# Optimization experiments

Hardware: AMD Instinct MI355X
Metric: run time of the kernel (lower is better)

Reference implementation:

```python
import jax, jax.numpy as jnp
import numpy as np

B, N, C, H = 4, 1024, 768, 12
D = C // H
HID = 4 * C
SCALE = D ** -0.5
EPS = 1e-6


def layernorm(x, w, b):
    mu = jnp.mean(x, axis=-1, keepdims=True)
    var = jnp.mean(jnp.square(x - mu), axis=-1, keepdims=True)
    return (x - mu) * jax.lax.rsqrt(var + EPS) * w + b


def setup_inputs() -> dict:
    key = jax.random.key(0)
    ks = jax.random.split(key, 16)
    s = lambda fan_in: 1.0 / np.sqrt(fan_in)
    return {
        "x": jax.random.normal(ks[0], (B, N, C), jnp.float32),
        "physics_bias": jax.random.normal(ks[1], (B, N, N), jnp.float32),
        "qkv_w": jax.random.normal(ks[2], (C, 3 * C), jnp.float32) * s(C),
        "qkv_b": jnp.zeros((3 * C,), jnp.float32),
        "proj_w": jax.random.normal(ks[3], (C, C), jnp.float32) * s(C),
        "proj_b": jnp.zeros((C,), jnp.float32),
        "n1_w": jnp.ones((C,), jnp.float32),
        "n1_b": jnp.zeros((C,), jnp.float32),
        "n2_w": jnp.ones((C,), jnp.float32),
        "n2_b": jnp.zeros((C,), jnp.float32),
        "fc1_w": jax.random.normal(ks[4], (C, HID), jnp.float32) * s(C),
        "fc1_b": jnp.zeros((HID,), jnp.float32),
        "fc2_w": jax.random.normal(ks[5], (HID, C), jnp.float32) * s(HID),
        "fc2_b": jnp.zeros((C,), jnp.float32),
    }


def reference(x, physics_bias, qkv_w, qkv_b, proj_w, proj_b,
              n1_w, n1_b, n2_w, n2_b, fc1_w, fc1_b, fc2_w, fc2_b):
    # --- biased self-attention (pre-norm) ---
    h = layernorm(x, n1_w, n1_b)                         # [B,N,C]
    qkv = (h @ qkv_w + qkv_b).reshape(B, N, 3, H, D)     # [B,N,3,H,D]
    q, k, v = (qkv[:, :, i] for i in range(3))           # each [B,N,H,D]
    attn = jnp.einsum('bnhd,bmhd->bhnm', q, k) * SCALE   # [B,H,N,N]
    attn = attn + physics_bias[:, None, :, :]            # additive physics bias
    attn = jax.nn.softmax(attn, axis=-1)
    o = jnp.einsum('bhnm,bmhd->bnhd', attn, v).reshape(B, N, C)
    x = x + (o @ proj_w + proj_b)
    # --- MLP (pre-norm) ---
    h = layernorm(x, n2_w, n2_b)
    h = jax.nn.gelu(h @ fc1_w + fc1_b, approximate=False)
    x = x + (h @ fc2_w + fc2_b)
    return x
```

## Files before the change

### kernel.cpp

```cpp
#include <hip/hip_runtime.h>
#include <hip/hip_bf16.h>
#include <cstdint>
#include <cstddef>

#define B_   4
#define N_   1024
#define C_   768
#define H_   12
#define D_   64
#define HID_ 3072
#define M_   4096

typedef __attribute__((ext_vector_type(8))) short short8;
typedef __attribute__((ext_vector_type(8))) unsigned short ushort8;
typedef __attribute__((ext_vector_type(4))) float f32x4;

__device__ __forceinline__ void gload16(const void* g, void* l) {
  __builtin_amdgcn_global_load_lds(
      (const __attribute__((address_space(1))) void*)g,
      (__attribute__((address_space(3))) void*)l, 16, 0, 0);
}

__device__ __forceinline__ unsigned short f2bf(float f) {
  __hip_bfloat16 h = __float2bfloat16(f);
  return __builtin_bit_cast(unsigned short, h);
}
__device__ __forceinline__ float bf2f(unsigned short u) {
  unsigned int x = ((unsigned int)u) << 16;
  return __builtin_bit_cast(float, x);
}
__device__ __forceinline__ float ex2(float x) {
  float r;
  asm("v_exp_f32 %0, %1" : "=v"(r) : "v"(x));
  return r;
}
__device__ __forceinline__ float frcp(float x) {
  float r;
  asm("v_rcp_f32 %0, %1" : "=v"(r) : "v"(x));
  return r;
}

__global__ __launch_bounds__(256) void wconv_all(
    const float* __restrict__ qkv_w, const float* __restrict__ proj_w,
    const float* __restrict__ fc1_w, const float* __restrict__ fc2_w,
    unsigned short* __restrict__ wt_qkv, unsigned short* __restrict__ wt_proj,
    unsigned short* __restrict__ wt_fc1, unsigned short* __restrict__ wt_fc2) {
  __shared__ float tile[32][33];
  const int bid = blockIdx.x;
  const float* W;
  unsigned short* Wt;
  int K, Nn, bx, by;
  if (bid < 1728) {
    W = qkv_w; Wt = wt_qkv; K = 768; Nn = 2304;
    bx = bid % 72; by = bid / 72;
  } else if (bid < 1728 + 576) {
    const int i = bid - 1728;
    W = proj_w; Wt = wt_proj; K = 768; Nn = 768;
    bx = i % 24; by = i / 24;
  } else if (bid < 1728 + 576 + 2304) {
    const int i = bid - (1728 + 576);
    W = fc1_w; Wt = wt_fc1; K = 768; Nn = 3072;
    bx = i % 96; by = i / 96;
  } else {
    const int i = bid - (1728 + 576 + 2304);
    W = fc2_w; Wt = wt_fc2; K = 3072; Nn = 768;
    bx = i % 24; by = i / 24;
  }
  const int tx = threadIdx.x & 31, ty = threadIdx.x >> 5;
  const int n0 = bx * 32, k0 = by * 32;
#pragma unroll
  for (int i = 0; i < 32; i += 8)
    tile[ty + i][tx] = W[(size_t)(k0 + ty + i) * Nn + n0 + tx];
  __syncthreads();
#pragma unroll
  for (int i = 0; i < 32; i += 8)
    Wt[(size_t)(n0 + ty + i) * K + k0 + tx] = f2bf(tile[tx][ty + i]);
}

__global__ __launch_bounds__(256) void ln_kernel(const float* __restrict__ x,
                                                 const float* __restrict__ w,
                                                 const float* __restrict__ b,
                                                 unsigned short* __restrict__ out) {
  __shared__ float sbuf[8];
  const int row = blockIdx.x;
  const int t = threadIdx.x;
  const float* xr = x + (size_t)row * C_;
  float v0 = xr[t], v1 = xr[t + 256], v2 = xr[t + 512];
  float s = v0 + v1 + v2;
  float ss = v0 * v0 + v1 * v1 + v2 * v2;
#pragma unroll
  for (int m = 32; m >= 1; m >>= 1) {
    s += __shfl_xor(s, m);
    ss += __shfl_xor(ss, m);
  }
  const int wave = t >> 6, lane = t & 63;
  if (lane == 0) { sbuf[wave] = s; sbuf[4 + wave] = ss; }
  __syncthreads();
  s = sbuf[0] + sbuf[1] + sbuf[2] + sbuf[3];
  ss = sbuf[4] + sbuf[5] + sbuf[6] + sbuf[7];
  const float mu = s * (1.f / C_);
  const float var = ss * (1.f / C_) - mu * mu;
  const float rstd = rsqrtf(var + 1e-6f);
  unsigned short* o = out + (size_t)row * C_;
  o[t]       = f2bf((v0 - mu) * rstd * w[t]       + b[t]);
  o[t + 256] = f2bf((v1 - mu) * rstd * w[t + 256] + b[t + 256]);
  o[t + 512] = f2bf((v2 - mu) * rstd * w[t + 512] + b[t + 512]);
}

template <int MF, bool GELU, bool RES, bool OUTF, bool OUTB>
__global__ __launch_bounds__(256) void gemm_bt(const unsigned short* __restrict__ A,
                                               const unsigned short* __restrict__ Bt,
                                               const float* __restrict__ bias,
                                               const float* __restrict__ res,
                                               float* __restrict__ outF,
                                               unsigned short* __restrict__ outB,
                                               int M, int Nn, int K) {
  __shared__ unsigned short As[3][MF * 32 * 32];
  __shared__ unsigned short Bs[3][128 * 32];
  const int t = threadIdx.x;
  const int lane = t & 63;
  const int wave = t >> 6;
  const int wm = wave >> 1, wn = wave & 1;
  const int r15 = lane & 15, g = lane >> 4;

  constexpr int SPX = (MF == 4) ? 4 : 8;
  constexpr int LGS = (MF == 4) ? 2 : 3;
  const int orig = blockIdx.y * gridDim.x + blockIdx.x;
  const int xcd = orig & 7;
  const int j = orig >> 3;
  const int bm = xcd * SPX + (j & (SPX - 1));
  const int bn = j >> LGS;

  f32x4 acc[MF][4];
#pragma unroll
  for (int m = 0; m < MF; ++m)
#pragma unroll
    for (int n = 0; n < 4; ++n) acc[m][n] = (f32x4){0.f, 0.f, 0.f, 0.f};

  const int srow = t >> 2;
  const int schunk = (t & 3) ^ ((t >> 3) & 3);
  const unsigned short* ga0 = A + (size_t)(bm * (MF * 32) + srow) * K + schunk * 8;
  const unsigned short* gb0 = Bt + (size_t)(bn * 128 + srow) * K + schunk * 8;

#define GSTAGE(kt_, buf_)                                                  \
  {                                                                        \
    const unsigned short* ga = ga0 + (kt_)*32;                             \
    const unsigned short* gb = gb0 + (kt_)*32;                             \
    gload16(ga, (char*)As[buf_] + wave * 1024);                            \
    if constexpr (MF == 4)                                                 \
      gload16(ga + (size_t)64 * K, (char*)As[buf_] + wave * 1024 + 4096);  \
    gload16(gb, (char*)Bs[buf_] + wave * 1024);                            \
    gload16(gb + (size_t)64 * K, (char*)Bs[buf_] + wave * 1024 + 4096);    \
  }

  const int nk = K >> 5;
  GSTAGE(0, 0);
  GSTAGE(1, 1);

  int arow[MF], aoff[MF], boff[4];
#pragma unroll
  for (int m = 0; m < MF; ++m) {
    arow[m] = wm * (MF * 16) + m * 16 + r15;
    aoff[m] = arow[m] * 32 + (g ^ ((arow[m] >> 1) & 3)) * 8;
  }
#pragma unroll
  for (int n = 0; n < 4; ++n) {
    const int rn = wn * 64 + n * 16 + r15;
    boff[n] = rn * 32 + (g ^ ((rn >> 1) & 3)) * 8;
  }

  int rd = 0;
  for (int kt = 0; kt < nk; ++kt) {
    const int rem = nk - kt;
    if (rem >= 2) {
      if constexpr (MF == 4) asm volatile("s_waitcnt vmcnt(4)" ::: "memory");
      else                   asm volatile("s_waitcnt vmcnt(3)" ::: "memory");
    } else {
      asm volatile("s_waitcnt vmcnt(0)" ::: "memory");
    }
    __builtin_amdgcn_s_barrier();

    short8 af[MF], bf[4];
#pragma unroll
    for (int m = 0; m < MF; ++m)
      af[m] = *(const short8*)(As[rd] + aoff[m]);
#pragma unroll
    for (int n = 0; n < 4; ++n)
      bf[n] = *(const short8*)(Bs[rd] + boff[n]);

    if (kt + 2 < nk) {
      const int wr = (rd + 2 >= 3) ? rd - 1 : rd + 2;
      GSTAGE(kt + 2, wr);
    }

    asm volatile("s_waitcnt lgkmcnt(0)" ::: "memory");
    __builtin_amdgcn_sched_barrier(0);
    __builtin_amdgcn_s_setprio(1);
#pragma unroll
    for (int m = 0; m < MF; ++m)
#pragma unroll
      for (int n = 0; n < 4; ++n)
        acc[m][n] = __builtin_amdgcn_mfma_f32_16x16x32_bf16(af[m], bf[n], acc[m][n], 0, 0, 0);
    __builtin_amdgcn_s_setprio(0);
    rd = (rd == 2) ? 0 : rd + 1;
  }
#undef GSTAGE

#pragma unroll
  for (int m = 0; m < MF; ++m) {
#pragma unroll
    for (int n = 0; n < 4; ++n) {
#pragma unroll
      for (int r = 0; r < 4; ++r) {
        const int row = bm * (MF * 32) + wm * (MF * 16) + m * 16 + g * 4 + r;
        const int col = bn * 128 + wn * 64 + n * 16 + r15;
        float v = acc[m][n][r] + bias[col];
        if (GELU) v = 0.5f * v * (1.f + erff(v * 0.70710678118654752f));
        if (RES) v += res[(size_t)row * Nn + col];
        if (OUTF) outF[(size_t)row * Nn + col] = v;
        if (OUTB) outB[(size_t)row * Nn + col] = f2bf(v);
      }
    }
  }
}

__global__ __launch_bounds__(256) void attn_kernel(const unsigned short* __restrict__ qkv,
                                                   const float* __restrict__ pbias,
                                                   unsigned short* __restrict__ o) {
  __shared__ unsigned short Ks[2][64 * 64];
  __shared__ unsigned short Vt[2][64 * 64];
  __shared__ unsigned short Ps[4][16 * 64];
  const int t = threadIdx.x, lane = t & 63, wave = t >> 6;
  const int bh = blockIdx.y;
  const int b = bh / H_, h = bh % H_;
  const int q0 = blockIdx.x * 64;
  const int r15 = lane & 15, g = lane >> 4;
  const int qrow = q0 + wave * 16;
  const float LOG2E = 1.44269504088896f;
  const float QS = 0.125f * 1.44269504088896f;
  const int NT = N_ / 64;

  short8 aq[2];
  {
    const unsigned short* qp =
        qkv + (size_t)(b * N_ + qrow + r15) * (3 * C_) + h * D_ + g * 8;
    const ushort8 r0 = *(const ushort8*)qp;
    const ushort8 r1 = *(const ushort8*)(qp + 32);
#pragma unroll
    for (int jj = 0; jj < 8; ++jj) {
      aq[0][jj] = (short)f2bf(bf2f(r0[jj]) * QS);
      aq[1][jj] = (short)f2bf(bf2f(r1[jj]) * QS);
    }
  }
  short8 ones;
#pragma unroll
  for (int jj = 0; jj < 8; ++jj) ones[jj] = (short)0x3F80;

  f32x4 oacc[4], lacc;
#pragma unroll
  for (int n = 0; n < 4; ++n) oacc[n] = (f32x4){0.f, 0.f, 0.f, 0.f};
  lacc = (f32x4){0.f, 0.f, 0.f, 0.f};
  float m_run = -1e30f;

  const unsigned short* kbase = qkv + (size_t)b * N_ * (3 * C_) + C_ + h * D_;
  const unsigned short* vbase = qkv + (size_t)b * N_ * (3 * C_) + 2 * C_ + h * D_;
  const float* bq = pbias + (size_t)b * N_ * N_ + (size_t)(qrow + r15) * N_;

  const int krow = t >> 3;
  const int kchunk = (t & 7) ^ (krow & 7);
  const int vp = t & 31;
  const int vq = t >> 5;
  const int vkey = vp * 2, vd0 = vq * 8;

#define KSTAGE(kb_, nb_)                                                       \
  {                                                                            \
    const unsigned short* kg =                                                 \
        kbase + (size_t)((kb_)*64 + krow) * (3 * C_) + kchunk * 8;             \
    gload16(kg, (char*)Ks[nb_] + wave * 1024);                                 \
    gload16(kg + (size_t)32 * (3 * C_), (char*)Ks[nb_] + wave * 1024 + 4096);  \
  }

#define VWRITE(nb_, va_, vb_)                                                        \
  {                                                                                  \
    char* vdst = (char*)Vt[nb_];                                                     \
    _Pragma("unroll") for (int jj = 0; jj < 8; ++jj) {                               \
      const int d = vd0 + jj;                                                        \
      const unsigned int pack =                                                      \
          (unsigned int)(va_)[jj] | ((unsigned int)(vb_)[jj] << 16);                 \
      *(unsigned int*)(vdst + d * 128 + (((vp >> 2) ^ (d & 7)) << 4) +               \
                       (vp & 3) * 4) = pack;                                         \
    }                                                                                \
  }

  KSTAGE(0, 0);
  f32x4 biasA[4], biasB[4];
  {
    const unsigned short* vg = vbase + (size_t)vkey * (3 * C_) + vd0;
    const ushort8 va0 = *(const ushort8*)vg;
    const ushort8 vb0 = *(const ushort8*)(vg + 3 * C_);
#pragma unroll
    for (int n = 0; n < 4; ++n) biasA[n] = *(const f32x4*)(bq + n * 16 + g * 4);
#pragma unroll
    for (int n = 0; n < 4; ++n) biasB[n] = *(const f32x4*)(bq + 64 + n * 16 + g * 4);
    VWRITE(0, va0, vb0);
  }

#define ABODY(kb_, BS)                                                             \
  {                                                                                \
    const int cur_ = (kb_)&1;                                                      \
    asm volatile("s_waitcnt lgkmcnt(0)" ::: "memory");                             \
    asm volatile("s_waitcnt vmcnt(4)" ::: "memory");                               \
    __builtin_amdgcn_s_barrier();                                                  \
    ushort8 va, vb2;                                                               \
    const bool more = (kb_) + 1 < NT;                                              \
    if (more) {                                                                    \
      KSTAGE((kb_) + 1, cur_ ^ 1);                                                 \
      const unsigned short* vg =                                                   \
          vbase + (size_t)(((kb_) + 1) * 64 + vkey) * (3 * C_) + vd0;              \
      va = *(const ushort8*)vg;                                                    \
      vb2 = *(const ushort8*)(vg + 3 * C_);                                        \
    }                                                                              \
    const unsigned short* Ksc = Ks[cur_];                                          \
    f32x4 sacc[4];                                                                 \
    _Pragma("unroll") for (int n = 0; n < 4; ++n)                                  \
        sacc[n] = (f32x4){0.f, 0.f, 0.f, 0.f};                                     \
    __builtin_amdgcn_s_setprio(1);                                                 \
    _Pragma("unroll") for (int kk = 0; kk < 2; ++kk) {                             \
      _Pragma("unroll") for (int n = 0; n < 4; ++n) {                              \
        short8 bk = *(const short8*)(Ksc + (n * 16 + r15) * 64 +                   \
                                     (((kk * 4 + g) ^ (r15 & 7)) << 3));           \
        sacc[n] =                                                                  \
            __builtin_amdgcn_mfma_f32_16x16x32_bf16(bk, aq[kk], sacc[n], 0, 0, 0); \
      }                                                                            \
    }                                                                              \
    __builtin_amdgcn_s_setprio(0);                                                 \
    float p[4][4];                                                                 \
    float tm = -3e38f;                                                             \
    _Pragma("unroll") for (int n = 0; n < 4; ++n) {                                \
      _Pragma("unroll") for (int r = 0; r < 4; ++r) {                              \
        p[n][r] = fmaf(BS[n][r], LOG2E, sacc[n][r]);                               \
        tm = fmaxf(tm, p[n][r]);                                                   \
      }                                                                            \
    }                                                                              \
    __builtin_amdgcn_sched_barrier(0);                                             \
    {                                                                              \
      const float* bsrc = bq + (((kb_) + 2 < NT ? (kb_) + 2 : NT - 1) << 6);       \
      _Pragma("unroll") for (int n = 0; n < 4; ++n)                                \
          BS[n] = *(const f32x4*)(bsrc + n * 16 + g * 4);                          \
    }                                                                              \
    __builtin_amdgcn_sched_barrier(0);                                             \
    tm = fmaxf(tm, __shfl_xor(tm, 16));                                            \
    tm = fmaxf(tm, __shfl_xor(tm, 32));                                            \
    const int need = (tm > m_run + 8.0f);                                          \
    if (__any(need)) {                                                             \
      const float mn = fmaxf(m_run, tm);                                           \
      const float corr = ex2(m_run - mn);                                          \
      m_run = mn;                                                                  \
      float cr[4];                                                                 \
      _Pragma("unroll") for (int r = 0; r < 4; ++r)                                \
          cr[r] = __shfl(corr, g * 4 + r);                                         \
      _Pragma("unroll") for (int r = 0; r < 4; ++r) {                              \
        lacc[r] *= cr[r];                                                          \
        _Pragma("unroll") for (int n = 0; n < 4; ++n) oacc[n][r] *= cr[r];         \
      }                                                                            \
    }                                                                              \
    _Pragma("unroll") for (int n = 0; n < 4; ++n) {                                \
      _Pragma("unroll") for (int r = 0; r < 4; ++r)                                \
          p[n][r] = ex2(p[n][r] - m_run);                                          \
    }                                                                              \
    unsigned short* Psw = Ps[wave];                                                \
    _Pragma("unroll") for (int n = 0; n < 4; ++n) {                                \
      _Pragma("unroll") for (int r = 0; r < 4; ++r) {                              \
        const int col = n * 16 + g * 4 + r;                                        \
        Psw[r15 * 64 + (((col >> 3) ^ (r15 & 7)) << 3) + (col & 7)] =              \
            f2bf(p[n][r]);                                                         \
      }                                                                            \
    }                                                                              \
    const unsigned short* Vtc = Vt[cur_];                                          \
    __builtin_amdgcn_s_setprio(1);                                                 \
    _Pragma("unroll") for (int kk = 0; kk < 2; ++kk) {                             \
      short8 ap =                                                                  \
          *(const short8*)(Psw + r15 * 64 + (((kk * 4 + g) ^ (r15 & 7)) << 3));    \
      lacc = __builtin_amdgcn_mfma_f32_16x16x32_bf16(ap, ones, lacc, 0, 0, 0);     \
      _Pragma("unroll") for (int n = 0; n < 4; ++n) {                              \
        short8 bv = *(const short8*)(Vtc + (n * 16 + r15) * 64 +                   \
                                     (((kk * 4 + g) ^ (r15 & 7)) << 3));           \
        oacc[n] =                                                                  \
            __builtin_amdgcn_mfma_f32_16x16x32_bf16(ap, bv, oacc[n], 0, 0, 0);     \
      }                                                                            \
    }                                                                              \
    __builtin_amdgcn_s_setprio(0);                                                 \
    if (more) { VWRITE(cur_ ^ 1, va, vb2); }                                       \
  }

  for (int kb2 = 0; kb2 < NT; kb2 += 2) {
    ABODY(kb2, biasA);
    ABODY(kb2 + 1, biasB);
  }
#undef ABODY
#undef KSTAGE
#undef VWRITE

  float rl[4];
#pragma unroll
  for (int r = 0; r < 4; ++r) rl[r] = frcp(lacc[r]);
#pragma unroll
  for (int n = 0; n < 4; ++n) {
#pragma unroll
    for (int r = 0; r < 4; ++r) {
      const int row = qrow + g * 4 + r;
      const float v = oacc[n][r] * rl[r];
      o[(size_t)(b * N_ + row) * C_ + h * D_ + n * 16 + r15] = f2bf(v);
    }
  }
}

extern "C" void kernel_launch(void* const* d_in, const int* in_sizes, int n_in,
                              void* d_out, int out_size, void* d_ws, size_t ws_size,
                              hipStream_t stream) {
  const float* x      = (const float*)d_in[0];
  const float* pbias  = (const float*)d_in[1];
  const float* qkv_w  = (const float*)d_in[2];
  const float* qkv_b  = (const float*)d_in[3];
  const float* proj_w = (const float*)d_in[4];
  const float* proj_b = (const float*)d_in[5];
  const float* n1_w   = (const float*)d_in[6];
  const float* n1_b   = (const float*)d_in[7];
  const float* n2_w   = (const float*)d_in[8];
  const float* n2_b   = (const float*)d_in[9];
  const float* fc1_w  = (const float*)d_in[10];
  const float* fc1_b  = (const float*)d_in[11];
  const float* fc2_w  = (const float*)d_in[12];
  const float* fc2_b  = (const float*)d_in[13];
  float* out = (float*)d_out;

  char* ws = (char*)d_ws;
  unsigned short* wt_qkv  = (unsigned short*)(ws + 0);
  unsigned short* wt_proj = (unsigned short*)(ws + 3538944);
  unsigned short* wt_fc1  = (unsigned short*)(ws + 4718592);
  unsigned short* wt_fc2  = (unsigned short*)(ws + 9437184);
  float*          x2      = (float*)(ws + 14155776);
  unsigned short* h1      = (unsigned short*)(ws + 26738688);
  unsigned short* qkvb    = (unsigned short*)(ws + 33030144);

  wconv_all<<<1728 + 576 + 2304 + 2304, 256, 0, stream>>>(
      qkv_w, proj_w, fc1_w, fc2_w, wt_qkv, wt_proj, wt_fc1, wt_fc2);

  ln_kernel<<<M_, 256, 0, stream>>>(x, n1_w, n1_b, h1);
  gemm_bt<4, false, false, false, true><<<dim3(32, 18), 256, 0, stream>>>(
      h1, wt_qkv, qkv_b, nullptr, nullptr, qkvb, M_, 3 * C_, C_);
  attn_kernel<<<dim3(N_ / 64, B_ * H_), 256, 0, stream>>>(qkvb, pbias, h1);
  gemm_bt<2, false, true, true, false><<<dim3(64, 6), 256, 0, stream>>>(
      h1, wt_proj, proj_b, x, x2, nullptr, M_, C_, C_);
  ln_kernel<<<M_, 256, 0, stream>>>(x2, n2_w, n2_b, h1);
  gemm_bt<4, true, false, false, true><<<dim3(32, 24), 256, 0, stream>>>(
      h1, wt_fc1, fc1_b, nullptr, nullptr, qkvb, M_, HID_, C_);
  gemm_bt<2, false, true, true, false><<<dim3(64, 6), 256, 0, stream>>>(
      qkvb, wt_fc2, fc2_b, x2, out, nullptr, M_, C_, HID_);
}
```

Before: 180.9 us.

## Load K tiles directly into registers instead of staging through LDS

The attention kernel now reads K fragments from global memory straight into MFMA operand registers (double-buffered KA/KB), removing the K shared-memory buffer and its async LDS loads. The physics-bias prefetch also changes from a two-ahead A/B scheme to a one-ahead bcur/bnext scheme issued alongside the K and V loads. This cuts LDS traffic and footprint but raises register pressure and makes each wave fetch K on its own, with less coalesced 16-byte global loads and no sharing of K across the four waves.

```diff
diff --git a/kernel.cpp b/kernel.cpp
--- a/kernel.cpp
+++ b/kernel.cpp
@@ -227,7 +227,6 @@
 __global__ __launch_bounds__(256) void attn_kernel(const unsigned short* __restrict__ qkv,
                                                    const float* __restrict__ pbias,
                                                    unsigned short* __restrict__ o) {
-  __shared__ unsigned short Ks[2][64 * 64];
   __shared__ unsigned short Vt[2][64 * 64];
   __shared__ unsigned short Ps[4][16 * 64];
   const int t = threadIdx.x, lane = t & 63, wave = t >> 6;
@@ -264,21 +263,18 @@
 
   const unsigned short* kbase = qkv + (size_t)b * N_ * (3 * C_) + C_ + h * D_;
   const unsigned short* vbase = qkv + (size_t)b * N_ * (3 * C_) + 2 * C_ + h * D_;
+  const unsigned short* kls = kbase + (size_t)r15 * (3 * C_) + g * 8;
   const float* bq = pbias + (size_t)b * N_ * N_ + (size_t)(qrow + r15) * N_;
 
-  const int krow = t >> 3;
-  const int kchunk = (t & 7) ^ (krow & 7);
   const int vp = t & 31;
   const int vq = t >> 5;
   const int vkey = vp * 2, vd0 = vq * 8;
 
-#define KSTAGE(kb_, nb_)                                                       \
-  {                                                                            \
-    const unsigned short* kg =                                                 \
-        kbase + (size_t)((kb_)*64 + krow) * (3 * C_) + kchunk * 8;             \
-    gload16(kg, (char*)Ks[nb_] + wave * 1024);                                 \
-    gload16(kg + (size_t)32 * (3 * C_), (char*)Ks[nb_] + wave * 1024 + 4096);  \
-  }
+#define KLOAD(kb_, DST)                                                        \
+  _Pragma("unroll") for (int kk = 0; kk < 2; ++kk)                             \
+      _Pragma("unroll") for (int n = 0; n < 4; ++n)                            \
+          DST[kk * 4 + n] = *(const short8*)(                                  \
+              kls + (size_t)((kb_)*64 + n * 16) * (3 * C_) + kk * 32);
 
 #define VWRITE(nb_, va_, vb_)                                                        \
   {                                                                                  \
@@ -292,45 +288,43 @@
     }                                                                                \
   }
 
-  KSTAGE(0, 0);
-  f32x4 biasA[4], biasB[4];
+  short8 KA[8], KB[8];
+  KLOAD(0, KA);
   {
     const unsigned short* vg = vbase + (size_t)vkey * (3 * C_) + vd0;
     const ushort8 va0 = *(const ushort8*)vg;
     const ushort8 vb0 = *(const ushort8*)(vg + 3 * C_);
-#pragma unroll
-    for (int n = 0; n < 4; ++n) biasA[n] = *(const f32x4*)(bq + n * 16 + g * 4);
-#pragma unroll
-    for (int n = 0; n < 4; ++n) biasB[n] = *(const f32x4*)(bq + 64 + n * 16 + g * 4);
     VWRITE(0, va0, vb0);
   }
-
-#define ABODY(kb_, BS)                                                             \
+  f32x4 bcur[4], bnext[4];
+#pragma unroll
+  for (int n = 0; n < 4; ++n)
+    bcur[n] = *(const f32x4*)(bq + n * 16 + g * 4);
+
+#define ABODY(kb_, KC, KN)                                                         \
   {                                                                                \
     const int cur_ = (kb_)&1;                                                      \
     asm volatile("s_waitcnt lgkmcnt(0)" ::: "memory");                             \
-    asm volatile("s_waitcnt vmcnt(4)" ::: "memory");                               \
     __builtin_amdgcn_s_barrier();                                                  \
     ushort8 va, vb2;                                                               \
     const bool more = (kb_) + 1 < NT;                                              \
     if (more) {                                                                    \
-      KSTAGE((kb_) + 1, cur_ ^ 1);                                                 \
+      KLOAD((kb_) + 1, KN);                                                        \
       const unsigned short* vg =                                                   \
           vbase + (size_t)(((kb_) + 1) * 64 + vkey) * (3 * C_) + vd0;              \
       va = *(const ushort8*)vg;                                                    \
       vb2 = *(const ushort8*)(vg + 3 * C_);                                        \
-    }                                                                              \
-    const unsigned short* Ksc = Ks[cur_];                                          \
+      _Pragma("unroll") for (int n = 0; n < 4; ++n)                                \
+          bnext[n] = *(const f32x4*)(bq + (((kb_) + 1) << 6) + n * 16 + g * 4);    \
+    }                                                                              \
     f32x4 sacc[4];                                                                 \
     _Pragma("unroll") for (int n = 0; n < 4; ++n)                                  \
         sacc[n] = (f32x4){0.f, 0.f, 0.f, 0.f};                                     \
     __builtin_amdgcn_s_setprio(1);                                                 \
     _Pragma("unroll") for (int kk = 0; kk < 2; ++kk) {                             \
       _Pragma("unroll") for (int n = 0; n < 4; ++n) {                              \
-        short8 bk = *(const short8*)(Ksc + (n * 16 + r15) * 64 +                   \
-                                     (((kk * 4 + g) ^ (r15 & 7)) << 3));           \
-        sacc[n] =                                                                  \
-            __builtin_amdgcn_mfma_f32_16x16x32_bf16(bk, aq[kk], sacc[n], 0, 0, 0); \
+        sacc[n] = __builtin_amdgcn_mfma_f32_16x16x32_bf16(KC[kk * 4 + n], aq[kk],  \
+                                                          sacc[n], 0, 0, 0);       \
       }                                                                            \
     }                                                                              \
     __builtin_amdgcn_s_setprio(0);                                                 \
@@ -338,17 +332,10 @@
     float tm = -3e38f;                                                             \
     _Pragma("unroll") for (int n = 0; n < 4; ++n) {                                \
       _Pragma("unroll") for (int r = 0; r < 4; ++r) {                              \
-        p[n][r] = fmaf(BS[n][r], LOG2E, sacc[n][r]);                               \
+        p[n][r] = fmaf(bcur[n][r], LOG2E, sacc[n][r]);                             \
         tm = fmaxf(tm, p[n][r]);                                                   \
       }                                                                            \
     }                                                                              \
-    __builtin_amdgcn_sched_barrier(0);                                             \
-    {                                                                              \
-      const float* bsrc = bq + (((kb_) + 2 < NT ? (kb_) + 2 : NT - 1) << 6);       \
-      _Pragma("unroll") for (int n = 0; n < 4; ++n)                                \
-          BS[n] = *(const f32x4*)(bsrc + n * 16 + g * 4);                          \
-    }                                                                              \
-    __builtin_amdgcn_sched_barrier(0);                                             \
     tm = fmaxf(tm, __shfl_xor(tm, 16));                                            \
     tm = fmaxf(tm, __shfl_xor(tm, 32));                                            \
     const int need = (tm > m_run + 8.0f);                                          \
@@ -390,15 +377,18 @@
       }                                                                            \
     }                                                                              \
     __builtin_amdgcn_s_setprio(0);                                                 \
-    if (more) { VWRITE(cur_ ^ 1, va, vb2); }                                       \
+    if (more) {                                                                    \
+      VWRITE(cur_ ^ 1, va, vb2);                                                   \
+      _Pragma("unroll") for (int n = 0; n < 4; ++n) bcur[n] = bnext[n];            \
+    }                                                                              \
   }
 
   for (int kb2 = 0; kb2 < NT; kb2 += 2) {
-    ABODY(kb2, biasA);
-    ABODY(kb2 + 1, biasB);
+    ABODY(kb2, KA, KB);
+    ABODY(kb2 + 1, KB, KA);
   }
 #undef ABODY
-#undef KSTAGE
+#undef KLOAD
 #undef VWRITE
 
   float rl[4];
```

Result: slower. 215.1 us (+18.9%).
